# Performance work log

Measured on AMD Instinct MI355X. Metric: run time of the kernel, lower is better.

## Reference

```python
import jax, jax.numpy as jnp
import numpy as np
from jax import lax
from jax.scipy.special import logsumexp

B, T, C, XD = 64, 8192, 16, 6
LOG2PI = float(np.log(2.0 * np.pi))


def setup_inputs() -> dict:
    key = jax.random.key(0)
    k1, k2, k3, k4, k5 = jax.random.split(key, 5)
    return {
        "x": jax.random.normal(k1, (B, T, XD), dtype=jnp.float32),
        "observation_means": jax.random.uniform(k2, (C, XD), dtype=jnp.float32),
        "observation_stddevs": jax.random.uniform(k3, (C, XD), dtype=jnp.float32),
        "log_A": jax.random.normal(k4, (C, C), dtype=jnp.float32),
        "log_pi": jax.random.normal(k5, (C,), dtype=jnp.float32),
    }


def _emission_logp(x, means, stds):
    # Normal(means[:, :4], relu(stds[:, :4]) + 0.1).log_prob(x[:, :, None, :4]).sum(-1)
    mu = means[:, :4]                         # [C,4]
    sigma = jax.nn.relu(stds[:, :4]) + 0.1    # [C,4]
    z = (x[:, :, None, :4] - mu) / sigma      # [B,T,C,4]
    lp = -0.5 * z * z - jnp.log(sigma) - 0.5 * LOG2PI
    return lp.sum(-1)                         # [B,T,C]


def _forward_backward(logp_tm, log_A, log_pi):
    # logp_tm: time-major [T,B,C]
    a0 = logp_tm[0] + log_pi                  # [B,C]
    s0 = logsumexp(a0, axis=-1)               # [B]
    alpha0 = a0 - s0[:, None]

    def fwd_step(alpha_prev, logp_t):
        a = logp_t + logsumexp(alpha_prev[:, :, None] + log_A[None], axis=1)
        s = logsumexp(a, axis=-1)
        alpha = a - s[:, None]
        return alpha, (alpha, s)

    _, (alphas, scalers) = lax.scan(fwd_step, alpha0, logp_tm[1:])
    log_alpha = jnp.concatenate([alpha0[None], alphas], axis=0)     # [T,B,C]
    log_scalers = jnp.concatenate([s0[None], scalers], axis=0)      # [T,B]

    beta_last = jnp.zeros_like(alpha0)

    def bwd_step(beta_next, inp):
        logp_t1, s_t = inp
        # torch: logsumexp(beta[t+1][:,:,None] + log_A[None] + logp[t+1][:,None,:], dim=-1)
        b = logsumexp(beta_next[:, :, None] + log_A[None] + logp_t1[:, None, :], axis=2)
        beta = b - s_t[:, None]
        return beta, beta

    _, betas = lax.scan(bwd_step, beta_last, (logp_tm[1:], log_scalers[:-1]), reverse=True)
    log_beta = jnp.concatenate([betas, beta_last[None]], axis=0)    # [T,B,C]

    log_gamma = log_alpha + log_beta
    logp_x = log_scalers.sum(axis=0)                                # [B]
    return log_alpha, log_beta, log_scalers, log_gamma, logp_x


def _viterbi(logp_tm, log_A, log_pi):
    d0 = logp_tm[0] + log_pi                  # [B,C]

    def vit_step(delta_prev, logp_t):
        scores = delta_prev[:, :, None] + log_A[None]   # [B,C,C]
        max_val = scores.max(axis=1)
        max_arg = scores.argmax(axis=1).astype(jnp.int32)
        delta = max_val + logp_t
        return delta, max_arg

    delta_last, psis = lax.scan(vit_step, d0, logp_tm[1:])  # psis: [T-1,B,C]
    c_last = jnp.argmax(delta_last, axis=-1).astype(jnp.int32)      # [B]

    def back_step(c_next, psi_t):
        c = jnp.take_along_axis(psi_t, c_next[:, None], axis=1)[:, 0]
        return c, c

    _, cs = lax.scan(back_step, c_last, psis, reverse=True)
    c = jnp.concatenate([cs, c_last[None]], axis=0)                 # [T,B]
    return jnp.swapaxes(c, 0, 1)                                    # [B,T]


def reference(x, observation_means, observation_stddevs, log_A, log_pi):
    logp_x_c = _emission_logp(x, observation_means, observation_stddevs)  # [B,T,C]
    logA = jax.nn.log_softmax(log_A, axis=1)
    logpi = jax.nn.log_softmax(log_pi, axis=0)
    logp_tm = jnp.swapaxes(logp_x_c, 0, 1)    # [T,B,C]
    _, _, _, _, logp_x = _forward_backward(logp_tm, logA, logpi)
    c_est = _viterbi(logp_tm, logA, logpi)
    return logp_x, c_est
```

## Files before the change

kernel.cpp:

```cpp
#include <hip/hip_runtime.h>
#include <stdint.h>
#include <stddef.h>

#define BB 64
#define TT 8192
#define CC 16
#define NBK 64
#define KBK 128

static __device__ __forceinline__ float groupMax16(float v) {
    v = fmaxf(v, __shfl_xor(v, 1, 16));
    v = fmaxf(v, __shfl_xor(v, 2, 16));
    v = fmaxf(v, __shfl_xor(v, 4, 16));
    v = fmaxf(v, __shfl_xor(v, 8, 16));
    return v;
}
static __device__ __forceinline__ float groupSum16(float v) {
    v += __shfl_xor(v, 1, 16);
    v += __shfl_xor(v, 2, 16);
    v += __shfl_xor(v, 4, 16);
    v += __shfl_xor(v, 8, 16);
    return v;
}

static __device__ __forceinline__ void bcast16(float v, float q[16]) {
#pragma unroll
    for (int j = 0; j < 16; ++j) q[j] = __shfl(v, j, 16);
}

struct MaxI { float v; int i; };
static __device__ __forceinline__ MaxI argmax16(const float s[16]) {
    float m1[8]; int i1[8];
#pragma unroll
    for (int j = 0; j < 8; ++j) {
        bool t = s[2*j] >= s[2*j+1];
        m1[j] = t ? s[2*j] : s[2*j+1];
        i1[j] = t ? 2*j : 2*j+1;
    }
    float m2[4]; int i2[4];
#pragma unroll
    for (int j = 0; j < 4; ++j) {
        bool t = m1[2*j] >= m1[2*j+1];
        m2[j] = t ? m1[2*j] : m1[2*j+1];
        i2[j] = t ? i1[2*j] : i1[2*j+1];
    }
    float m3[2]; int i3[2];
#pragma unroll
    for (int j = 0; j < 2; ++j) {
        bool t = m2[2*j] >= m2[2*j+1];
        m3[j] = t ? m2[2*j] : m2[2*j+1];
        i3[j] = t ? i2[2*j] : i2[2*j+1];
    }
    bool t = m3[0] >= m3[1];
    MaxI r; r.v = t ? m3[0] : m3[1]; r.i = t ? i3[0] : i3[1];
    return r;
}

__global__ __launch_bounds__(256) void k_emis(
    const float* __restrict__ x, const float* __restrict__ mug,
    const float* __restrict__ sdg, float* __restrict__ LP, float* __restrict__ M)
{
    const int tid = threadIdx.x;
    const int c = tid & 15, tl = tid >> 4;
    const int b = blockIdx.x >> 9;
    const int t = ((blockIdx.x & 511) << 4) + tl;

    const float mu0 = mug[c*6+0], mu1 = mug[c*6+1], mu2 = mug[c*6+2], mu3 = mug[c*6+3];
    const float s0 = fmaxf(sdg[c*6+0], 0.f) + 0.1f;
    const float s1 = fmaxf(sdg[c*6+1], 0.f) + 0.1f;
    const float s2 = fmaxf(sdg[c*6+2], 0.f) + 0.1f;
    const float s3 = fmaxf(sdg[c*6+3], 0.f) + 0.1f;

    const float* xp = x + ((size_t)b*TT + t)*6;
    const float x0 = xp[0], x1 = xp[1], x2 = xp[2], x3 = xp[3];
    const float z0 = (x0-mu0)/s0, z1 = (x1-mu1)/s1, z2 = (x2-mu2)/s2, z3 = (x3-mu3)/s3;
    const float HL2P = 0.91893853320467274178f;
    float e0 = -0.5f*(z0*z0) - logf(s0) - HL2P;
    float e1 = -0.5f*(z1*z1) - logf(s1) - HL2P;
    float e2 = -0.5f*(z2*z2) - logf(s2) - HL2P;
    float e3 = -0.5f*(z3*z3) - logf(s3) - HL2P;
    float lp = ((e0+e1)+e2)+e3;
    float m = groupMax16(lp);
    LP[((size_t)b*TT + t)*16 + c] = lp;
    if (c == 0) M[(size_t)b*TT + t] = m;
}

__global__ __launch_bounds__(64) void k_chain(
    const float* __restrict__ lAg, const float* __restrict__ lpig,
    const float* __restrict__ LP, const float* __restrict__ M,
    float* __restrict__ outLogp, uint32_t* __restrict__ PSI, int* __restrict__ CL)
{
    const int tid = threadIdx.x;
    const int g = tid >> 4, c = tid & 15;
    const bool isF = blockIdx.x < 16;
    const int b = ((int)(blockIdx.x & 15))*4 + g;

    float la[16];
#pragma unroll
    for (int j = 0; j < 16; ++j) {
        float raw = lAg[j*16 + c];
        float mx = groupMax16(raw);
        float sh = raw - mx;
        float sm = groupSum16(expf(sh));
        la[j] = sh - logf(sm);
    }
    float lpi;
    {
        float raw = lpig[c];
        float mx = groupMax16(raw);
        float sh = raw - mx;
        float sm = groupSum16(expf(sh));
        lpi = sh - logf(sm);
    }

    const float* lpb = LP + ((size_t)b*TT)*16 + c;
    const float LOG2E = 1.44269504088896340736f;

    if (isF) {
        float Ac[16];
#pragma unroll
        for (int j = 0; j < 16; ++j) Ac[j] = expf(la[j]);
        const float* mb = M + (size_t)b*TT;
        double macc = 0.0, lacc = 0.0;
        float q[16];

        auto fstep = [&](float lp, float m, bool renorm) {
            float p = exp2f((lp - m) * LOG2E);
            macc += (double)m;
            float a0 = q[0]*Ac[0];   a0 = fmaf(q[1],Ac[1],a0);   a0 = fmaf(q[2],Ac[2],a0);   a0 = fmaf(q[3],Ac[3],a0);
            float a1 = q[4]*Ac[4];   a1 = fmaf(q[5],Ac[5],a1);   a1 = fmaf(q[6],Ac[6],a1);   a1 = fmaf(q[7],Ac[7],a1);
            float a2 = q[8]*Ac[8];   a2 = fmaf(q[9],Ac[9],a2);   a2 = fmaf(q[10],Ac[10],a2); a2 = fmaf(q[11],Ac[11],a2);
            float a3 = q[12]*Ac[12]; a3 = fmaf(q[13],Ac[13],a3); a3 = fmaf(q[14],Ac[14],a3); a3 = fmaf(q[15],Ac[15],a3);
            float v = (a0 + a1) + (a2 + a3);
            if (renorm) {
                float S = ((q[0]+q[1])+(q[2]+q[3])) + ((q[4]+q[5])+(q[6]+q[7]))
                        + ((q[8]+q[9])+(q[10]+q[11])) + ((q[12]+q[13])+(q[14]+q[15]));
                lacc += (double)log2f(S);
                v *= __builtin_amdgcn_rcpf(S);
            }
            float av = p * v;
            bcast16(av, q);
        };

        {
            float lp = lpb[0], m = mb[0];
            float p = exp2f((lp - m) * LOG2E);
            macc += (double)m;
            float av = p * expf(lpi);
            bcast16(av, q);
        }
        fstep(lpb[1*16], mb[1], false);
        fstep(lpb[2*16], mb[2], false);
        fstep(lpb[3*16], mb[3], false);

        float clp0 = lpb[4*16], clp1 = lpb[5*16], clp2 = lpb[6*16], clp3 = lpb[7*16];
        float cm0 = mb[4], cm1 = mb[5], cm2 = mb[6], cm3 = mb[7];
        for (int t4 = 1; t4 < 2048; ++t4) {
            int nt = (t4 < 2047) ? 4*t4 + 4 : 4*t4;
            float nlp0 = lpb[(size_t)(nt+0)*16], nlp1 = lpb[(size_t)(nt+1)*16];
            float nlp2 = lpb[(size_t)(nt+2)*16], nlp3 = lpb[(size_t)(nt+3)*16];
            float nm0 = mb[nt+0], nm1 = mb[nt+1], nm2 = mb[nt+2], nm3 = mb[nt+3];
            fstep(clp0, cm0, true);
            fstep(clp1, cm1, false);
            fstep(clp2, cm2, false);
            fstep(clp3, cm3, false);
            clp0 = nlp0; clp1 = nlp1; clp2 = nlp2; clp3 = nlp3;
            cm0 = nm0; cm1 = nm1; cm2 = nm2; cm3 = nm3;
        }
        float S = ((q[0]+q[1])+(q[2]+q[3])) + ((q[4]+q[5])+(q[6]+q[7]))
                + ((q[8]+q[9])+(q[10]+q[11])) + ((q[12]+q[13])+(q[14]+q[15]));
        double logp = macc + 0.69314718055994530942 * (lacc + (double)log2f(S));
        if (c == 0) outLogp[b] = (float)logp;
    } else {
        float delta = lpb[0] + lpi;
        uint32_t* psib = PSI + (size_t)b*2048*16 + c;

        auto vstep = [&](float lp) -> int {
            float qd[16];
            bcast16(delta, qd);
            float s[16];
#pragma unroll
            for (int j = 0; j < 16; ++j) s[j] = qd[j] + la[j];
            MaxI r = argmax16(s);
            delta = r.v + lp;
            return r.i;
        };

        int a1 = vstep(lpb[1*16]);
        int a2 = vstep(lpb[2*16]);
        int a3 = vstep(lpb[3*16]);
        psib[0] = ((uint32_t)a1 << 8) | ((uint32_t)a2 << 16) | ((uint32_t)a3 << 24);

        float clp0 = lpb[4*16], clp1 = lpb[5*16], clp2 = lpb[6*16], clp3 = lpb[7*16];
        for (int t4 = 1; t4 < 2048; ++t4) {
            int nt = (t4 < 2047) ? 4*t4 + 4 : 4*t4;
            float nlp0 = lpb[(size_t)(nt+0)*16], nlp1 = lpb[(size_t)(nt+1)*16];
            float nlp2 = lpb[(size_t)(nt+2)*16], nlp3 = lpb[(size_t)(nt+3)*16];
            int b0 = vstep(clp0);
            int b1 = vstep(clp1);
            int b2 = vstep(clp2);
            int b3 = vstep(clp3);
            psib[(size_t)t4*16] = (uint32_t)b0 | ((uint32_t)b1 << 8)
                                | ((uint32_t)b2 << 16) | ((uint32_t)b3 << 24);
            clp0 = nlp0; clp1 = nlp1; clp2 = nlp2; clp3 = nlp3;
        }
        float qd[16];
        bcast16(delta, qd);
        MaxI r = argmax16(qd);
        if (c == 0) CL[b] = r.i;
    }
}

__global__ __launch_bounds__(64) void k_btA(const uint32_t* __restrict__ PSI,
                                            uint8_t* __restrict__ G)
{
    const int tid = threadIdx.x, gl = tid >> 4, c = tid & 15;
    const int gid = blockIdx.x*4 + gl;
    const int b = gid >> 6, i = gid & 63;
    __shared__ uint32_t lds[4][33][16];
    const uint32_t* psib = PSI + (size_t)b*2048*16;
    for (int s = 0; s < 33; ++s) {
        int t4 = 32*i + s; if (t4 > 2047) t4 = 2047;
        lds[gl][s][c] = psib[(size_t)t4*16 + c];
    }
    __syncthreads();
    const int lo = 128*i;
    const int hi = (i == 63) ? 8190 : lo + 127;
    int gg = c;
    for (int k = hi; k >= lo; --k) {
        int t = k + 1;
        uint32_t w = lds[gl][(t >> 2) - 32*i][gg];
        gg = (w >> ((t & 3)*8)) & 15;
    }
    G[((size_t)b*64 + i)*16 + c] = (uint8_t)gg;
}

__global__ __launch_bounds__(64) void k_btB(const uint8_t* __restrict__ G,
                                            const int* __restrict__ CL,
                                            uint8_t* __restrict__ BD)
{
    __shared__ uint8_t gl[64*64*16];
    const int tid = threadIdx.x;
    const uint4* src = (const uint4*)G;
    uint4* dst = (uint4*)gl;
    for (int k = 0; k < 64; ++k) dst[tid + 64*k] = src[tid + 64*k];
    __syncthreads();
    int b = tid;
    int e = CL[b];
    for (int i = 63; i >= 0; --i) {
        e = gl[((b*64) + i)*16 + e];
        BD[b*64 + i] = (uint8_t)e;
    }
}

__global__ __launch_bounds__(64) void k_btC(const uint32_t* __restrict__ PSI,
                                            const uint8_t* __restrict__ BD,
                                            const int* __restrict__ CL,
                                            float* __restrict__ oc)
{
    const int tid = threadIdx.x, gl = tid >> 4, c = tid & 15;
    const int gid = blockIdx.x*4 + gl;
    const int b = gid >> 6, i = gid & 63;
    __shared__ uint32_t lds[4][33][16];
    const uint32_t* psib = PSI + (size_t)b*2048*16;
    for (int s = 0; s < 33; ++s) {
        int t4 = 32*i + s; if (t4 > 2047) t4 = 2047;
        lds[gl][s][c] = psib[(size_t)t4*16 + c];
    }
    __syncthreads();
    const int lo = 128*i;
    const int hi = (i == 63) ? 8190 : lo + 127;
    int cn = (i == 63) ? CL[b] : (int)BD[b*64 + i + 1];
    float* ob = oc + (size_t)b*TT;
    if (i == 63 && c == 0) ob[8191] = (float)cn;
    for (int k = hi; k >= lo; --k) {
        int t = k + 1;
        uint32_t w = lds[gl][(t >> 2) - 32*i][cn];
        cn = (w >> ((t & 3)*8)) & 15;
        if (c == 0) ob[k] = (float)cn;
    }
}

extern "C" void kernel_launch(void* const* d_in, const int* in_sizes, int n_in,
                              void* d_out, int out_size, void* d_ws, size_t ws_size,
                              hipStream_t stream)
{
    (void)in_sizes; (void)n_in; (void)out_size; (void)ws_size;
    const float* x    = (const float*)d_in[0];
    const float* mug  = (const float*)d_in[1];
    const float* sdg  = (const float*)d_in[2];
    const float* lAg  = (const float*)d_in[3];
    const float* lpig = (const float*)d_in[4];
    float* out = (float*)d_out;

    uint8_t* ws = (uint8_t*)d_ws;
    uint32_t* PSI = (uint32_t*)(ws + 0);
    float* LP = (float*)(ws + (8ull << 20));
    float* M  = (float*)(ws + (40ull << 20));
    uint8_t* G  = ws + (42ull << 20);
    uint8_t* BD = G + 64*64*16;
    int* CL = (int*)(BD + 64*64);

    hipLaunchKernelGGL(k_emis, dim3(BB*TT/16), dim3(256), 0, stream, x, mug, sdg, LP, M);
    hipLaunchKernelGGL(k_chain, dim3(32), dim3(64), 0, stream, lAg, lpig, LP, M, out, PSI, CL);
    hipLaunchKernelGGL(k_btA, dim3(BB*NBK/4), dim3(64), 0, stream, PSI, G);
    hipLaunchKernelGGL(k_btB, dim3(1), dim3(64), 0, stream, G, CL, BD);
    hipLaunchKernelGGL(k_btC, dim3(BB*NBK/4), dim3(64), 0, stream, PSI, BD, CL, out + BB);
}
```

Measured before the change: 2.240 ms.

## Run one chain per wavefront and broadcast state via readlane instead of shuffles

The forward and Viterbi chain kernel now gives each batch row its own block, using only 16 active lanes, instead of packing four rows per wavefront. This lets the per-step broadcast of the 16-state vector use scalar readlane rather than ds_bpermute-based shuffles. The shuffles add LDS-path latency to every step of the serial recurrence. The LP/M prefetch is also deepened to two groups of four timesteps ahead. In exchange the kernel launches four times as many blocks, each using a quarter of a wavefront's lanes.

```diff
diff --git a/kernel.cpp b/kernel.cpp
--- a/kernel.cpp
+++ b/kernel.cpp
@@ -23,10 +23,7 @@
     return v;
 }
 
-static __device__ __forceinline__ void bcast16(float v, float q[16]) {
-#pragma unroll
-    for (int j = 0; j < 16; ++j) q[j] = __shfl(v, j, 16);
-}
+#define RL(v, j) __int_as_float(__builtin_amdgcn_readlane(__float_as_int(v), (j)))
 
 struct MaxI { float v; int i; };
 static __device__ __forceinline__ MaxI argmax16(const float s[16]) {
@@ -91,9 +88,10 @@
     float* __restrict__ outLogp, uint32_t* __restrict__ PSI, int* __restrict__ CL)
 {
     const int tid = threadIdx.x;
-    const int g = tid >> 4, c = tid & 15;
-    const bool isF = blockIdx.x < 16;
-    const int b = ((int)(blockIdx.x & 15))*4 + g;
+    if (tid >= 16) return;
+    const int c = tid;
+    const bool isF = blockIdx.x < 64;
+    const int b = (int)(blockIdx.x & 63);
 
     float la[16];
 #pragma unroll
@@ -122,9 +120,19 @@
         for (int j = 0; j < 16; ++j) Ac[j] = expf(la[j]);
         const float* mb = M + (size_t)b*TT;
         double macc = 0.0, lacc = 0.0;
+        float av;
         float q[16];
 
+        {
+            float lp = lpb[0], m = mb[0];
+            float p = exp2f((lp - m) * LOG2E);
+            macc += (double)m;
+            av = p * expf(lpi);
+        }
+
         auto fstep = [&](float lp, float m, bool renorm) {
+#pragma unroll
+            for (int j = 0; j < 16; ++j) q[j] = RL(av, j);
             float p = exp2f((lp - m) * LOG2E);
             macc += (double)m;
             float a0 = q[0]*Ac[0];   a0 = fmaf(q[1],Ac[1],a0);   a0 = fmaf(q[2],Ac[2],a0);   a0 = fmaf(q[3],Ac[3],a0);
@@ -138,35 +146,33 @@
                 lacc += (double)log2f(S);
                 v *= __builtin_amdgcn_rcpf(S);
             }
-            float av = p * v;
-            bcast16(av, q);
+            av = p * v;
         };
 
-        {
-            float lp = lpb[0], m = mb[0];
-            float p = exp2f((lp - m) * LOG2E);
-            macc += (double)m;
-            float av = p * expf(lpi);
-            bcast16(av, q);
-        }
         fstep(lpb[1*16], mb[1], false);
         fstep(lpb[2*16], mb[2], false);
         fstep(lpb[3*16], mb[3], false);
 
-        float clp0 = lpb[4*16], clp1 = lpb[5*16], clp2 = lpb[6*16], clp3 = lpb[7*16];
-        float cm0 = mb[4], cm1 = mb[5], cm2 = mb[6], cm3 = mb[7];
+        float clp[4], cmv[4], nlp[4], nmv[4];
+#pragma unroll
+        for (int j = 0; j < 4; ++j) { clp[j] = lpb[(size_t)(4+j)*16]; cmv[j] = mb[4+j]; }
+#pragma unroll
+        for (int j = 0; j < 4; ++j) { nlp[j] = lpb[(size_t)(8+j)*16]; nmv[j] = mb[8+j]; }
+
         for (int t4 = 1; t4 < 2048; ++t4) {
-            int nt = (t4 < 2047) ? 4*t4 + 4 : 4*t4;
-            float nlp0 = lpb[(size_t)(nt+0)*16], nlp1 = lpb[(size_t)(nt+1)*16];
-            float nlp2 = lpb[(size_t)(nt+2)*16], nlp3 = lpb[(size_t)(nt+3)*16];
-            float nm0 = mb[nt+0], nm1 = mb[nt+1], nm2 = mb[nt+2], nm3 = mb[nt+3];
-            fstep(clp0, cm0, true);
-            fstep(clp1, cm1, false);
-            fstep(clp2, cm2, false);
-            fstep(clp3, cm3, false);
-            clp0 = nlp0; clp1 = nlp1; clp2 = nlp2; clp3 = nlp3;
-            cm0 = nm0; cm1 = nm1; cm2 = nm2; cm3 = nm3;
+            int pt = (t4 + 2 < 2048) ? t4 + 2 : 2047;
+            float tlp[4], tmv[4];
+#pragma unroll
+            for (int j = 0; j < 4; ++j) { tlp[j] = lpb[(size_t)(4*pt+j)*16]; tmv[j] = mb[4*pt+j]; }
+            fstep(clp[0], cmv[0], true);
+            fstep(clp[1], cmv[1], false);
+            fstep(clp[2], cmv[2], false);
+            fstep(clp[3], cmv[3], false);
+#pragma unroll
+            for (int j = 0; j < 4; ++j) { clp[j] = nlp[j]; cmv[j] = nmv[j]; nlp[j] = tlp[j]; nmv[j] = tmv[j]; }
         }
+#pragma unroll
+        for (int j = 0; j < 16; ++j) q[j] = RL(av, j);
         float S = ((q[0]+q[1])+(q[2]+q[3])) + ((q[4]+q[5])+(q[6]+q[7]))
                 + ((q[8]+q[9])+(q[10]+q[11])) + ((q[12]+q[13])+(q[14]+q[15]));
         double logp = macc + 0.69314718055994530942 * (lacc + (double)log2f(S));
@@ -177,7 +183,8 @@
 
         auto vstep = [&](float lp) -> int {
             float qd[16];
-            bcast16(delta, qd);
+#pragma unroll
+            for (int j = 0; j < 16; ++j) qd[j] = RL(delta, j);
             float s[16];
 #pragma unroll
             for (int j = 0; j < 16; ++j) s[j] = qd[j] + la[j];
@@ -191,21 +198,29 @@
         int a3 = vstep(lpb[3*16]);
         psib[0] = ((uint32_t)a1 << 8) | ((uint32_t)a2 << 16) | ((uint32_t)a3 << 24);
 
-        float clp0 = lpb[4*16], clp1 = lpb[5*16], clp2 = lpb[6*16], clp3 = lpb[7*16];
+        float clp[4], nlp[4];
+#pragma unroll
+        for (int j = 0; j < 4; ++j) clp[j] = lpb[(size_t)(4+j)*16];
+#pragma unroll
+        for (int j = 0; j < 4; ++j) nlp[j] = lpb[(size_t)(8+j)*16];
+
         for (int t4 = 1; t4 < 2048; ++t4) {
-            int nt = (t4 < 2047) ? 4*t4 + 4 : 4*t4;
-            float nlp0 = lpb[(size_t)(nt+0)*16], nlp1 = lpb[(size_t)(nt+1)*16];
-            float nlp2 = lpb[(size_t)(nt+2)*16], nlp3 = lpb[(size_t)(nt+3)*16];
-            int b0 = vstep(clp0);
-            int b1 = vstep(clp1);
-            int b2 = vstep(clp2);
-            int b3 = vstep(clp3);
+            int pt = (t4 + 2 < 2048) ? t4 + 2 : 2047;
+            float tlp[4];
+#pragma unroll
+            for (int j = 0; j < 4; ++j) tlp[j] = lpb[(size_t)(4*pt+j)*16];
+            int b0 = vstep(clp[0]);
+            int b1 = vstep(clp[1]);
+            int b2 = vstep(clp[2]);
+            int b3 = vstep(clp[3]);
             psib[(size_t)t4*16] = (uint32_t)b0 | ((uint32_t)b1 << 8)
                                 | ((uint32_t)b2 << 16) | ((uint32_t)b3 << 24);
-            clp0 = nlp0; clp1 = nlp1; clp2 = nlp2; clp3 = nlp3;
+#pragma unroll
+            for (int j = 0; j < 4; ++j) { clp[j] = nlp[j]; nlp[j] = tlp[j]; }
         }
         float qd[16];
-        bcast16(delta, qd);
+#pragma unroll
+        for (int j = 0; j < 16; ++j) qd[j] = RL(delta, j);
         MaxI r = argmax16(qd);
         if (c == 0) CL[b] = r.i;
     }
@@ -302,7 +317,7 @@
     int* CL = (int*)(BD + 64*64);
 
     hipLaunchKernelGGL(k_emis, dim3(BB*TT/16), dim3(256), 0, stream, x, mug, sdg, LP, M);
-    hipLaunchKernelGGL(k_chain, dim3(32), dim3(64), 0, stream, lAg, lpig, LP, M, out, PSI, CL);
+    hipLaunchKernelGGL(k_chain, dim3(128), dim3(64), 0, stream, lAg, lpig, LP, M, out, PSI, CL);
     hipLaunchKernelGGL(k_btA, dim3(BB*NBK/4), dim3(64), 0, stream, PSI, G);
     hipLaunchKernelGGL(k_btB, dim3(1), dim3(64), 0, stream, G, CL, BD);
     hipLaunchKernelGGL(k_btC, dim3(BB*NBK/4), dim3(64), 0, stream, PSI, BD, CL, out + BB);
```

New measurement: 3.236 ms. 44.5% more time.
